# Kernel tuning notes

Measured on AMD Instinct MI355X. Metric: run time of the kernel, lower is better.

The kernel has to match this reference:

```python
import jax, jax.numpy as jnp
import numpy as np

NUM_USER = 50000
NUM_ITEM = 30000
N_NODES = NUM_USER + NUM_ITEM
N_EDGES = 1_000_000
FEAT_DIM = 768
DIM_LATENT = 128
DIM_ID = 64
NEG_SLOPE = 0.01  # F.leaky_relu default


def leaky_relu(x):
    return jnp.where(x >= 0, x, NEG_SLOPE * x)


def l2_normalize(x, eps=1e-12):
    # F.normalize(dim=-1): divide by clamped L2 norm
    n = jnp.sqrt(jnp.sum(x * x, axis=-1, keepdims=True))
    return x / jnp.maximum(n, eps)


def graph_gat(x, W, edge_index, num_nodes):
    """MGAT GraphGAT: x -> x@W, gated inner-product attention, softmax over
    incoming edges per destination node, scatter-add, L2 normalize."""
    x = x @ W                                    # [N, D]
    src = edge_index[0]                          # j (source)
    dst = edge_index[1]                          # i (target)
    x_j = x[src]                                 # [E, D]
    x_i = x[dst]                                 # [E, D]
    inner = jnp.sum(x_i * x_j, axis=-1)          # [E]
    # gate: sigmoid(deg(src)^-0.5 * inner)
    deg = jax.ops.segment_sum(jnp.ones_like(inner), src, num_segments=num_nodes)
    gate = jax.nn.sigmoid(deg[src] ** -0.5 * inner)
    score = inner * gate                         # [E]
    # segment softmax over destination nodes
    smax = jax.ops.segment_max(score, dst, num_segments=num_nodes)
    e = jnp.exp(score - smax[dst])
    denom = jax.ops.segment_sum(e, dst, num_segments=num_nodes)
    alpha = e / (denom[dst] + 1e-16)             # [E]
    out = jax.ops.segment_sum(x_j * alpha[:, None], dst, num_segments=num_nodes)
    return l2_normalize(out)


def setup_inputs() -> dict:
    key = jax.random.key(0)
    ks = jax.random.split(key, 16)

    def xavier(k, shape):
        fan_in, fan_out = shape[0], shape[1]
        std = float(np.sqrt(2.0 / (fan_in + fan_out)))
        return jax.random.normal(k, shape, dtype=jnp.float32) * std

    features = jax.random.normal(ks[0], (NUM_ITEM, FEAT_DIM), dtype=jnp.float32)
    id_embedding = jax.random.normal(ks[1], (N_NODES, DIM_ID), dtype=jnp.float32)
    # edge_index [2, E] with no self-loops (remove_self_loops is then identity)
    src = jax.random.randint(ks[2], (N_EDGES,), 0, N_NODES)
    off = jax.random.randint(ks[3], (N_EDGES,), 1, N_NODES)
    dst = (src + off) % N_NODES
    edge_index = jnp.stack([src, dst]).astype(jnp.int64)

    return {
        "features": features,
        "id_embedding": id_embedding,
        "edge_index": edge_index,
        "preference": xavier(ks[4], (NUM_USER, DIM_LATENT)),
        "mlp_w": xavier(ks[5], (FEAT_DIM, DIM_LATENT)),
        "mlp_b": jnp.zeros((DIM_LATENT,), dtype=jnp.float32),
        "conv1_w": xavier(ks[6], (DIM_LATENT, DIM_LATENT)),
        "lin1_w": xavier(ks[7], (DIM_LATENT, DIM_ID)),
        "lin1_b": jnp.zeros((DIM_ID,), dtype=jnp.float32),
        "g1_w": xavier(ks[8], (DIM_LATENT, DIM_ID)),
        "g1_b": jnp.zeros((DIM_ID,), dtype=jnp.float32),
        "conv2_w": xavier(ks[9], (DIM_ID, DIM_ID)),
        "lin2_w": xavier(ks[10], (DIM_ID, DIM_ID)),
        "lin2_b": jnp.zeros((DIM_ID,), dtype=jnp.float32),
        "g2_w": xavier(ks[11], (DIM_ID, DIM_ID)),
        "g2_b": jnp.zeros((DIM_ID,), dtype=jnp.float32),
    }


def reference(features, id_embedding, edge_index, preference, mlp_w, mlp_b,
              conv1_w, lin1_w, lin1_b, g1_w, g1_b,
              conv2_w, lin2_w, lin2_b, g2_w, g2_b):
    temp_features = jnp.tanh(features @ mlp_w + mlp_b)        # [num_item, dim_latent]
    x = jnp.concatenate([preference, temp_features], axis=0)  # [N, dim_latent]
    x = l2_normalize(x)

    h = leaky_relu(graph_gat(x, conv1_w, edge_index, N_NODES))
    x_hat = leaky_relu(x @ lin1_w + lin1_b) + id_embedding
    x1 = leaky_relu(h @ g1_w + g1_b + x_hat)                  # [N, dim_id]

    h = leaky_relu(graph_gat(x1, conv2_w, edge_index, N_NODES))
    x_hat = leaky_relu(x1 @ lin2_w + lin2_b) + id_embedding
    x2 = leaky_relu(h @ g2_w + g2_b + x_hat)                  # [N, dim_id]

    return jnp.concatenate([x1, x2], axis=1)                  # [N, 2*dim_id]
```

## Files before the change

kernel.cpp:

```cpp
#include <hip/hip_runtime.h>
#include <hip/hip_bf16.h>
#include <math.h>

#define NUM_USER 50000
#define NUM_ITEM 30000
#define N_NODES  80000
#define N_EDGES  1000000
#define FEAT_DIM 768
#define DLAT 128
#define DID  64
#define NEG_SLOPE 0.01f

#define SCAN_NB ((N_NODES + 255) / 256)

__device__ __forceinline__ float leaky(float v) { return v >= 0.f ? v : NEG_SLOPE * v; }

__device__ __forceinline__ float wave_reduce_sum(float v) {
#pragma unroll
    for (int off = 32; off > 0; off >>= 1) v += __shfl_xor(v, off, 64);
    return v;
}

__device__ __forceinline__ unsigned short f2bf(float f) {
    unsigned int u = __float_as_uint(f);
    unsigned int r = u + 0x7fffu + ((u >> 16) & 1u);
    return (unsigned short)(r >> 16);
}
__device__ __forceinline__ float bf2f(unsigned short h) {
    return __uint_as_float(((unsigned int)h) << 16);
}

typedef __attribute__((ext_vector_type(8))) short short8v;
typedef __attribute__((ext_vector_type(4))) float f32x4;

__device__ __forceinline__ void split_store8(
    float4 a, float4 b, unsigned short* dh, unsigned short* dl)
{
    float v[8] = {a.x, a.y, a.z, a.w, b.x, b.y, b.z, b.w};
    unsigned int ph[4], pl[4];
#pragma unroll
    for (int i = 0; i < 4; i++) {
        unsigned short h0 = f2bf(v[2*i]),   l0 = f2bf(v[2*i]   - bf2f(h0));
        unsigned short h1 = f2bf(v[2*i+1]), l1 = f2bf(v[2*i+1] - bf2f(h1));
        ph[i] = (unsigned int)h0 | ((unsigned int)h1 << 16);
        pl[i] = (unsigned int)l0 | ((unsigned int)l1 << 16);
    }
    *(int4*)dh = make_int4((int)ph[0], (int)ph[1], (int)ph[2], (int)ph[3]);
    *(int4*)dl = make_int4((int)pl[0], (int)pl[1], (int)pl[2], (int)pl[3]);
}

template<int KK, int NN>
__global__ __launch_bounds__(256) void wt_prep_g_kernel(
    const float* __restrict__ W, unsigned short* __restrict__ Wh,
    unsigned short* __restrict__ Wl)
{
    int id = blockIdx.x * 256 + threadIdx.x;
    if (id < KK * NN) {
        int n = id / KK, k = id % KK;
        float v = W[(size_t)k * NN + n];
        unsigned short h = f2bf(v);
        Wh[id] = h;
        Wl[id] = f2bf(v - bf2f(h));
    }
}

template<int K, int NC>
__global__ __launch_bounds__(256) void conv_mfma_kernel(
    const float* __restrict__ X, int ldx,
    const unsigned short* __restrict__ Wth, const unsigned short* __restrict__ Wtl,
    float* __restrict__ O, int ldo)
{
    constexpr int NW = NC / 64;
    constexpr int MW = 4 / NW;
    constexpr int WROWS = 64 / MW;
    constexpr int MF = WROWS / 16;
    constexpr int KSTEPS = K / 32;
    constexpr int KP = K + 8;

    __shared__ unsigned short sAh[64][KP];
    __shared__ unsigned short sAl[64][KP];

    const int tid = threadIdx.x;
    const int lane = tid & 63;
    const int w = tid >> 6;
    const int wr = w / NW, wc = w % NW;
    const int r0 = blockIdx.x * 64;

#pragma unroll
    for (int it = 0; it < K / 32; it++) {
        int slot = tid + it * 256;
        int row = slot / (K / 8);
        int k8 = (slot % (K / 8)) * 8;
        const float4* p = (const float4*)(X + (size_t)(r0 + row) * ldx + k8);
        split_store8(p[0], p[1], &sAh[row][k8], &sAl[row][k8]);
    }
    __syncthreads();

    f32x4 acc[MF][4];
#pragma unroll
    for (int m = 0; m < MF; m++)
#pragma unroll
        for (int n = 0; n < 4; n++) acc[m][n] = (f32x4){0.f, 0.f, 0.f, 0.f};

#pragma unroll
    for (int ks = 0; ks < KSTEPS; ks++) {
        int klane = ks * 32 + (lane >> 4) * 8;
        short8v ah[MF], al[MF];
#pragma unroll
        for (int m = 0; m < MF; m++) {
            int row = wr * WROWS + m * 16 + (lane & 15);
            ah[m] = *(const short8v*)&sAh[row][klane];
            al[m] = *(const short8v*)&sAl[row][klane];
        }
#pragma unroll
        for (int n = 0; n < 4; n++) {
            int col = wc * 64 + n * 16 + (lane & 15);
            short8v bh = *(const short8v*)(Wth + (size_t)col * K + klane);
            short8v bl = *(const short8v*)(Wtl + (size_t)col * K + klane);
#pragma unroll
            for (int m = 0; m < MF; m++) {
                acc[m][n] = __builtin_amdgcn_mfma_f32_16x16x32_bf16(ah[m], bh, acc[m][n], 0, 0, 0);
                acc[m][n] = __builtin_amdgcn_mfma_f32_16x16x32_bf16(ah[m], bl, acc[m][n], 0, 0, 0);
                acc[m][n] = __builtin_amdgcn_mfma_f32_16x16x32_bf16(al[m], bh, acc[m][n], 0, 0, 0);
            }
        }
    }

#pragma unroll
    for (int m = 0; m < MF; m++) {
        int rbase = r0 + wr * WROWS + m * 16 + (lane >> 4) * 4;
#pragma unroll
        for (int n = 0; n < 4; n++) {
            int col = wc * 64 + n * 16 + (lane & 15);
#pragma unroll
            for (int q = 0; q < 4; q++)
                O[(size_t)(rbase + q) * ldo + col] = acc[m][n][q];
        }
    }
}

template<int K>
__global__ __launch_bounds__(256) void combine_mfma_kernel(
    const float* __restrict__ H, int ldh,
    const float* __restrict__ X, int ldx,
    const unsigned short* __restrict__ Gth, const unsigned short* __restrict__ Gtl,
    const unsigned short* __restrict__ Lth, const unsigned short* __restrict__ Ltl,
    const float* __restrict__ g_b, const float* __restrict__ lin_b,
    const float* __restrict__ id_emb, float* __restrict__ out, int out_off)
{
    constexpr int KSTEPS = K / 32;
    constexpr int KP = K + 8;

    __shared__ unsigned short sHh[64][KP];
    __shared__ unsigned short sHl[64][KP];
    __shared__ unsigned short sXh[64][KP];
    __shared__ unsigned short sXl[64][KP];

    const int tid = threadIdx.x;
    const int lane = tid & 63;
    const int wr = tid >> 6;
    const int r0 = blockIdx.x * 64;

#pragma unroll
    for (int it = 0; it < K / 32; it++) {
        int slot = tid + it * 256;
        int row = slot / (K / 8);
        int k8 = (slot % (K / 8)) * 8;
        const float4* ph = (const float4*)(H + (size_t)(r0 + row) * ldh + k8);
        split_store8(ph[0], ph[1], &sHh[row][k8], &sHl[row][k8]);
        const float4* px = (const float4*)(X + (size_t)(r0 + row) * ldx + k8);
        split_store8(px[0], px[1], &sXh[row][k8], &sXl[row][k8]);
    }
    __syncthreads();

    f32x4 accG[4], accL[4];
#pragma unroll
    for (int n = 0; n < 4; n++) {
        accG[n] = (f32x4){0.f, 0.f, 0.f, 0.f};
        accL[n] = (f32x4){0.f, 0.f, 0.f, 0.f};
    }

#pragma unroll
    for (int ks = 0; ks < KSTEPS; ks++) {
        int klane = ks * 32 + (lane >> 4) * 8;
        int row = wr * 16 + (lane & 15);
        short8v hh = *(const short8v*)&sHh[row][klane];
        short8v hl = *(const short8v*)&sHl[row][klane];
        short8v xh = *(const short8v*)&sXh[row][klane];
        short8v xl = *(const short8v*)&sXl[row][klane];
#pragma unroll
        for (int n = 0; n < 4; n++) {
            int col = n * 16 + (lane & 15);
            short8v gh = *(const short8v*)(Gth + (size_t)col * K + klane);
            short8v gl = *(const short8v*)(Gtl + (size_t)col * K + klane);
            short8v lh = *(const short8v*)(Lth + (size_t)col * K + klane);
            short8v ll = *(const short8v*)(Ltl + (size_t)col * K + klane);
            accG[n] = __builtin_amdgcn_mfma_f32_16x16x32_bf16(hh, gh, accG[n], 0, 0, 0);
            accG[n] = __builtin_amdgcn_mfma_f32_16x16x32_bf16(hh, gl, accG[n], 0, 0, 0);
            accG[n] = __builtin_amdgcn_mfma_f32_16x16x32_bf16(hl, gh, accG[n], 0, 0, 0);
            accL[n] = __builtin_amdgcn_mfma_f32_16x16x32_bf16(xh, lh, accL[n], 0, 0, 0);
            accL[n] = __builtin_amdgcn_mfma_f32_16x16x32_bf16(xh, ll, accL[n], 0, 0, 0);
            accL[n] = __builtin_amdgcn_mfma_f32_16x16x32_bf16(xl, lh, accL[n], 0, 0, 0);
        }
    }

    int rbase = r0 + wr * 16 + (lane >> 4) * 4;
#pragma unroll
    for (int n = 0; n < 4; n++) {
        int col = n * 16 + (lane & 15);
        float gb = g_b[col], lb = lin_b[col];
#pragma unroll
        for (int q = 0; q < 4; q++) {
            int gr = rbase + q;
            float xhv = leaky(accL[n][q] + lb) + id_emb[(size_t)gr * DID + col];
            float v = leaky(accG[n][q] + gb + xhv);
            out[(size_t)gr * (2 * DID) + out_off + col] = v;
        }
    }
}

__global__ __launch_bounds__(256) void mlp_mfma_kernel(
    const float* __restrict__ F,
    const unsigned short* __restrict__ Wh, const unsigned short* __restrict__ Wl,
    const float* __restrict__ bias, float* __restrict__ xout)
{
    __shared__ unsigned short sAh[64][72];
    __shared__ unsigned short sAl[64][72];
    __shared__ unsigned short sWh[128][72];
    __shared__ unsigned short sWlo[128][72];

    const int tid = threadIdx.x;
    const int lane = tid & 63;
    const int w = tid >> 6;
    const int wr = w >> 1, wc = w & 1;
    const int r0 = blockIdx.x * 64;

    f32x4 acc[2][4];
#pragma unroll
    for (int m = 0; m < 2; m++)
#pragma unroll
        for (int n = 0; n < 4; n++) acc[m][n] = (f32x4){0.f, 0.f, 0.f, 0.f};

    for (int kc = 0; kc < FEAT_DIM; kc += 64) {
#pragma unroll
        for (int it = 0; it < 2; it++) {
            int slot = tid + it * 256;
            int row = slot >> 3;
            int k8 = (slot & 7) * 8;
            int gr = r0 + row;
            float4 a = make_float4(0.f, 0.f, 0.f, 0.f), b = a;
            if (gr < NUM_ITEM) {
                const float4* p = (const float4*)(F + (size_t)gr * FEAT_DIM + kc + k8);
                a = p[0]; b = p[1];
            }
            split_store8(a, b, &sAh[row][k8], &sAl[row][k8]);
        }
#pragma unroll
        for (int it = 0; it < 4; it++) {
            int slot = tid + it * 256;
            int n = slot >> 3;
            int k8 = (slot & 7) * 8;
            *(int4*)&sWh[n][k8]  = *(const int4*)(Wh + (size_t)n * FEAT_DIM + kc + k8);
            *(int4*)&sWlo[n][k8] = *(const int4*)(Wl + (size_t)n * FEAT_DIM + kc + k8);
        }
        __syncthreads();

#pragma unroll
        for (int k0 = 0; k0 < 64; k0 += 32) {
            int klane = k0 + (lane >> 4) * 8;
            short8v ah[2], al[2], bh[4], bl[4];
#pragma unroll
            for (int m = 0; m < 2; m++) {
                int row = wr * 32 + m * 16 + (lane & 15);
                ah[m] = *(const short8v*)&sAh[row][klane];
                al[m] = *(const short8v*)&sAl[row][klane];
            }
#pragma unroll
            for (int n = 0; n < 4; n++) {
                int col = wc * 64 + n * 16 + (lane & 15);
                bh[n] = *(const short8v*)&sWh[col][klane];
                bl[n] = *(const short8v*)&sWlo[col][klane];
            }
#pragma unroll
            for (int m = 0; m < 2; m++)
#pragma unroll
                for (int n = 0; n < 4; n++) {
                    acc[m][n] = __builtin_amdgcn_mfma_f32_16x16x32_bf16(ah[m], bh[n], acc[m][n], 0, 0, 0);
                    acc[m][n] = __builtin_amdgcn_mfma_f32_16x16x32_bf16(ah[m], bl[n], acc[m][n], 0, 0, 0);
                    acc[m][n] = __builtin_amdgcn_mfma_f32_16x16x32_bf16(al[m], bh[n], acc[m][n], 0, 0, 0);
                }
        }
        __syncthreads();
    }

#pragma unroll
    for (int m = 0; m < 2; m++) {
        int rbase = r0 + wr * 32 + m * 16 + (lane >> 4) * 4;
#pragma unroll
        for (int n = 0; n < 4; n++) {
            int col = wc * 64 + n * 16 + (lane & 15);
            float bv = bias[col];
#pragma unroll
            for (int q = 0; q < 4; q++) {
                int gr = rbase + q;
                if (gr < NUM_ITEM)
                    xout[(size_t)gr * DLAT + col] = tanhf(acc[m][n][q] + bv);
            }
        }
    }
}

__global__ __launch_bounds__(256) void l2norm_rows_kernel(float* __restrict__ x)
{
    int wid = blockIdx.x * 4 + (threadIdx.x >> 6);
    if (wid >= N_NODES) return;
    int lane = threadIdx.x & 63;
    float* row = x + (size_t)wid * DLAT;
    float v0 = row[lane], v1 = row[lane + 64];
    float s = wave_reduce_sum(v0 * v0 + v1 * v1);
    float inv = 1.0f / fmaxf(sqrtf(s), 1e-12f);
    row[lane] = v0 * inv;
    row[lane + 64] = v1 * inv;
}

__global__ __launch_bounds__(256) void count_kernel(
    const int* __restrict__ src, const int* __restrict__ dst,
    int* __restrict__ deg_out, int* __restrict__ cnt_in)
{
    int e = blockIdx.x * 256 + threadIdx.x;
    if (e < N_EDGES) {
        atomicAdd(&deg_out[src[e]], 1);
        atomicAdd(&cnt_in[dst[e]], 1);
    }
}

__global__ __launch_bounds__(256) void scan_local_kernel(
    const int* __restrict__ cnt, int* __restrict__ rowptr, int* __restrict__ blocksum)
{
    __shared__ int wsum[4];
    int gid = blockIdx.x * 256 + threadIdx.x;
    int lane = threadIdx.x & 63, w = threadIdx.x >> 6;
    int orig = (gid < N_NODES) ? cnt[gid] : 0;
    int v = orig;
#pragma unroll
    for (int off = 1; off < 64; off <<= 1) {
        int u = __shfl_up(v, off, 64);
        if (lane >= off) v += u;
    }
    if (lane == 63) wsum[w] = v;
    __syncthreads();
    int woff = 0;
#pragma unroll
    for (int i = 0; i < 4; i++) woff += (i < w) ? wsum[i] : 0;
    if (gid < N_NODES) rowptr[gid] = v - orig + woff;
    if (threadIdx.x == 255) blocksum[blockIdx.x] = woff + v;
}

__global__ __launch_bounds__(512) void scan_blocksums_kernel(int* __restrict__ blocksum)
{
    __shared__ int s[512];
    int t = threadIdx.x;
    int orig = (t < SCAN_NB) ? blocksum[t] : 0;
    s[t] = orig;
    __syncthreads();
    for (int off = 1; off < 512; off <<= 1) {
        int u = (t >= off) ? s[t - off] : 0;
        __syncthreads();
        s[t] += u;
        __syncthreads();
    }
    if (t < SCAN_NB) blocksum[t] = s[t] - orig;
}

__global__ __launch_bounds__(256) void scan_add_kernel(
    int* __restrict__ rowptr, const int* __restrict__ blocksum)
{
    int gid = blockIdx.x * 256 + threadIdx.x;
    if (gid < N_NODES) rowptr[gid] += blocksum[blockIdx.x];
    if (gid == 0) rowptr[N_NODES] = N_EDGES;
}

__global__ __launch_bounds__(256) void csr_fill_kernel(
    const int* __restrict__ src, const int* __restrict__ dst,
    const int* __restrict__ rowptr, int* __restrict__ cursor, int* __restrict__ csr_src)
{
    int e = blockIdx.x * 256 + threadIdx.x;
    if (e < N_EDGES) {
        int d = dst[e];
        int slot = rowptr[d] + atomicAdd(&cursor[d], 1);
        csr_src[slot] = src[e];
    }
}

__global__ __launch_bounds__(256) void deg_rsqrt_kernel(
    const int* __restrict__ deg_out, float* __restrict__ rsq)
{
    int n = blockIdx.x * 256 + threadIdx.x;
    if (n < N_NODES) rsq[n] = rsqrtf((float)deg_out[n]);
}

template<int D>
__global__ __launch_bounds__(256) void gat_layer_kernel(
    const float* __restrict__ xw, const int* __restrict__ rowptr,
    const int* __restrict__ csr_src, const float* __restrict__ rsq_deg,
    float* __restrict__ h)
{
    constexpr int SG  = D / 8;
    constexpr int EPC = 64 / SG;
    int wid = blockIdx.x * 4 + (threadIdx.x >> 6);
    if (wid >= N_NODES) return;
    const int lane = threadIdx.x & 63;
    const int g = lane / SG;
    const int t = lane % SG;
    const int start = rowptr[wid], end = rowptr[wid + 1];

    const float* xdp = xw + (size_t)wid * D + 8 * t;
    float4 xd0 = *(const float4*)(xdp);
    float4 xd1 = *(const float4*)(xdp + 4);

    float m = -1e30f, l = 0.f;
    float acc[8];
#pragma unroll
    for (int c = 0; c < 8; c++) acc[c] = 0.f;

    for (int base = start; base < end; base += EPC) {
        int i = base + g;
        bool valid = (i < end);
        int s = valid ? csr_src[i] : 0;
        const float* row = xw + (size_t)s * D + 8 * t;
        float4 a0 = *(const float4*)(row);
        float4 a1 = *(const float4*)(row + 4);
        float p = a0.x * xd0.x + a0.y * xd0.y + a0.z * xd0.z + a0.w * xd0.w
                + a1.x * xd1.x + a1.y * xd1.y + a1.z * xd1.z + a1.w * xd1.w;
#pragma unroll
        for (int off = SG / 2; off > 0; off >>= 1) p += __shfl_xor(p, off, 64);
        float rsd = valid ? rsq_deg[s] : 1.f;
        float gate = 1.0f / (1.0f + __expf(-(p * rsd)));
        float sc = valid ? p * gate : -1e30f;
        float mnew = fmaxf(m, sc);
        float scale = __expf(m - mnew);
        float w = valid ? __expf(sc - mnew) : 0.f;
        l = l * scale + w;
        acc[0] = acc[0] * scale + w * a0.x;
        acc[1] = acc[1] * scale + w * a0.y;
        acc[2] = acc[2] * scale + w * a0.z;
        acc[3] = acc[3] * scale + w * a0.w;
        acc[4] = acc[4] * scale + w * a1.x;
        acc[5] = acc[5] * scale + w * a1.y;
        acc[6] = acc[6] * scale + w * a1.z;
        acc[7] = acc[7] * scale + w * a1.w;
        m = mnew;
    }

#pragma unroll
    for (int off = SG; off < 64; off <<= 1) {
        float mo = __shfl_xor(m, off, 64);
        float lo = __shfl_xor(l, off, 64);
        float mnew = fmaxf(m, mo);
        float s1 = __expf(m - mnew), s2 = __expf(mo - mnew);
        l = l * s1 + lo * s2;
#pragma unroll
        for (int c = 0; c < 8; c++) {
            float ao = __shfl_xor(acc[c], off, 64);
            acc[c] = acc[c] * s1 + ao * s2;
        }
        m = mnew;
    }

    float invl = 1.0f / (l + 1e-16f);
    float ss = 0.f;
#pragma unroll
    for (int c = 0; c < 8; c++) { acc[c] *= invl; ss += acc[c] * acc[c]; }
#pragma unroll
    for (int off = SG / 2; off > 0; off >>= 1) ss += __shfl_xor(ss, off, 64);
    float inv = 1.0f / fmaxf(sqrtf(ss), 1e-12f);

    if (g == 0) {
        float4 o0, o1;
        o0.x = leaky(acc[0] * inv); o0.y = leaky(acc[1] * inv);
        o0.z = leaky(acc[2] * inv); o0.w = leaky(acc[3] * inv);
        o1.x = leaky(acc[4] * inv); o1.y = leaky(acc[5] * inv);
        o1.z = leaky(acc[6] * inv); o1.w = leaky(acc[7] * inv);
        float* op = h + (size_t)wid * D + 8 * t;
        *(float4*)(op) = o0;
        *(float4*)(op + 4) = o1;
    }
}

extern "C" void kernel_launch(void* const* d_in, const int* in_sizes, int n_in,
                              void* d_out, int out_size, void* d_ws, size_t ws_size,
                              hipStream_t stream)
{
    const float* features = (const float*)d_in[0];
    const float* id_emb   = (const float*)d_in[1];
    const int*   ei       = (const int*)d_in[2];
    const float* pref     = (const float*)d_in[3];
    const float* mlp_w    = (const float*)d_in[4];
    const float* mlp_b    = (const float*)d_in[5];
    const float* conv1_w  = (const float*)d_in[6];
    const float* lin1_w   = (const float*)d_in[7];
    const float* lin1_b   = (const float*)d_in[8];
    const float* g1_w     = (const float*)d_in[9];
    const float* g1_b     = (const float*)d_in[10];
    const float* conv2_w  = (const float*)d_in[11];
    const float* lin2_w   = (const float*)d_in[12];
    const float* lin2_b   = (const float*)d_in[13];
    const float* g2_w     = (const float*)d_in[14];
    const float* g2_b     = (const float*)d_in[15];
    const int* src = ei;
    const int* dst = ei + N_EDGES;
    float* out = (float*)d_out;

    float* x       = (float*)d_ws;
    float* xw      = x   + (size_t)N_NODES * DLAT;
    float* gat     = xw  + (size_t)N_NODES * DLAT;
    int*   deg_out = (int*)(gat + (size_t)N_NODES * DLAT);
    int*   cnt     = deg_out + N_NODES;
    int*   rowptr  = cnt + N_NODES;
    int*   csr_src = rowptr + N_NODES + 1;
    int*   blocksum = csr_src + N_EDGES;
    float* rsq_deg = (float*)cnt;
    unsigned short* mlpWh = (unsigned short*)gat;
    unsigned short* mlpWl = mlpWh + (size_t)FEAT_DIM * DLAT;
    unsigned short* wbase = (unsigned short*)(
        (((uintptr_t)(blocksum + SCAN_NB)) + 15) & ~(uintptr_t)15);
    unsigned short* wc1h = wbase;
    unsigned short* wc1l = wc1h + 16384;
    unsigned short* wl1h = wc1l + 16384;
    unsigned short* wl1l = wl1h + 8192;
    unsigned short* wg1h = wl1l + 8192;
    unsigned short* wg1l = wg1h + 8192;
    unsigned short* wc2h = wg1l + 8192;
    unsigned short* wc2l = wc2h + 4096;
    unsigned short* wl2h = wc2l + 4096;
    unsigned short* wl2l = wl2h + 4096;
    unsigned short* wg2h = wl2l + 4096;
    unsigned short* wg2l = wg2h + 4096;

    wt_prep_g_kernel<FEAT_DIM, DLAT><<<384, 256, 0, stream>>>(mlp_w, mlpWh, mlpWl);
    wt_prep_g_kernel<DLAT, DLAT><<<64, 256, 0, stream>>>(conv1_w, wc1h, wc1l);
    wt_prep_g_kernel<DLAT, DID><<<32, 256, 0, stream>>>(lin1_w, wl1h, wl1l);
    wt_prep_g_kernel<DLAT, DID><<<32, 256, 0, stream>>>(g1_w, wg1h, wg1l);
    wt_prep_g_kernel<DID, DID><<<16, 256, 0, stream>>>(conv2_w, wc2h, wc2l);
    wt_prep_g_kernel<DID, DID><<<16, 256, 0, stream>>>(lin2_w, wl2h, wl2l);
    wt_prep_g_kernel<DID, DID><<<16, 256, 0, stream>>>(g2_w, wg2h, wg2l);

    hipMemsetAsync(deg_out, 0, N_NODES * sizeof(int), stream);
    hipMemsetAsync(cnt, 0, N_NODES * sizeof(int), stream);
    count_kernel<<<(N_EDGES + 255) / 256, 256, 0, stream>>>(src, dst, deg_out, cnt);
    scan_local_kernel<<<SCAN_NB, 256, 0, stream>>>(cnt, rowptr, blocksum);
    scan_blocksums_kernel<<<1, 512, 0, stream>>>(blocksum);
    scan_add_kernel<<<SCAN_NB, 256, 0, stream>>>(rowptr, blocksum);
    hipMemsetAsync(cnt, 0, N_NODES * sizeof(int), stream);
    csr_fill_kernel<<<(N_EDGES + 255) / 256, 256, 0, stream>>>(src, dst, rowptr, cnt, csr_src);
    deg_rsqrt_kernel<<<(N_NODES + 255) / 256, 256, 0, stream>>>(deg_out, rsq_deg);

    hipMemcpyAsync(x, pref, (size_t)NUM_USER * DLAT * sizeof(float),
                   hipMemcpyDeviceToDevice, stream);
    mlp_mfma_kernel<<<(NUM_ITEM + 63) / 64, 256, 0, stream>>>(
        features, mlpWh, mlpWl, mlp_b, x + (size_t)NUM_USER * DLAT);
    l2norm_rows_kernel<<<(N_NODES + 3) / 4, 256, 0, stream>>>(x);

    conv_mfma_kernel<DLAT, DLAT><<<N_NODES / 64, 256, 0, stream>>>(
        x, DLAT, wc1h, wc1l, xw, DLAT);
    gat_layer_kernel<DLAT><<<(N_NODES + 3) / 4, 256, 0, stream>>>(
        xw, rowptr, csr_src, rsq_deg, gat);
    combine_mfma_kernel<DLAT><<<N_NODES / 64, 256, 0, stream>>>(
        gat, DLAT, x, DLAT, wg1h, wg1l, wl1h, wl1l, g1_b, lin1_b, id_emb, out, 0);

    conv_mfma_kernel<DID, DID><<<N_NODES / 64, 256, 0, stream>>>(
        out, 2 * DID, wc2h, wc2l, xw, DID);
    gat_layer_kernel<DID><<<(N_NODES + 3) / 4, 256, 0, stream>>>(
        xw, rowptr, csr_src, rsq_deg, gat);
    combine_mfma_kernel<DID><<<N_NODES / 64, 256, 0, stream>>>(
        gat, DID, out, 2 * DID, wg2h, wg2l, wl2h, wl2l, g2_b, lin2_b, id_emb, out, DID);
}
```

Baseline: 517.8 us.

## Store projected node features in bf16 and fuse small setup kernels

Measured after the change: 488.7 us. -5.6%, faster.

```diff
diff --git a/kernel.cpp b/kernel.cpp
--- a/kernel.cpp
+++ b/kernel.cpp
@@ -33,6 +33,14 @@
 typedef __attribute__((ext_vector_type(8))) short short8v;
 typedef __attribute__((ext_vector_type(4))) float f32x4;
 
+__device__ __forceinline__ void unpack8(int4 v, float* f) {
+    unsigned int u;
+    u = (unsigned int)v.x; f[0] = __uint_as_float(u << 16); f[1] = __uint_as_float(u & 0xFFFF0000u);
+    u = (unsigned int)v.y; f[2] = __uint_as_float(u << 16); f[3] = __uint_as_float(u & 0xFFFF0000u);
+    u = (unsigned int)v.z; f[4] = __uint_as_float(u << 16); f[5] = __uint_as_float(u & 0xFFFF0000u);
+    u = (unsigned int)v.w; f[6] = __uint_as_float(u << 16); f[7] = __uint_as_float(u & 0xFFFF0000u);
+}
+
 __device__ __forceinline__ void split_store8(
     float4 a, float4 b, unsigned short* dh, unsigned short* dl)
 {
@@ -49,26 +57,44 @@
     *(int4*)dl = make_int4((int)pl[0], (int)pl[1], (int)pl[2], (int)pl[3]);
 }
 
-template<int KK, int NN>
-__global__ __launch_bounds__(256) void wt_prep_g_kernel(
-    const float* __restrict__ W, unsigned short* __restrict__ Wh,
-    unsigned short* __restrict__ Wl)
+__device__ __forceinline__ void prep_one(int id, const float* W, int KK, int NN,
+                                         unsigned short* Wh, unsigned short* Wl)
+{
+    int n = id / KK, k = id - n * KK;
+    float v = W[(size_t)k * NN + n];
+    unsigned short h = f2bf(v);
+    Wh[id] = h;
+    Wl[id] = f2bf(v - bf2f(h));
+}
+
+__global__ __launch_bounds__(256) void wt_prep_all_kernel(
+    const float* __restrict__ mlp_w, const float* __restrict__ c1,
+    const float* __restrict__ l1, const float* __restrict__ g1,
+    const float* __restrict__ c2, const float* __restrict__ l2,
+    const float* __restrict__ g2,
+    unsigned short* __restrict__ mlpWh, unsigned short* __restrict__ mlpWl,
+    unsigned short* __restrict__ wc1h, unsigned short* __restrict__ wc1l,
+    unsigned short* __restrict__ wl1h, unsigned short* __restrict__ wl1l,
+    unsigned short* __restrict__ wg1h, unsigned short* __restrict__ wg1l,
+    unsigned short* __restrict__ wc2h, unsigned short* __restrict__ wc2l,
+    unsigned short* __restrict__ wl2h, unsigned short* __restrict__ wl2l,
+    unsigned short* __restrict__ wg2h, unsigned short* __restrict__ wg2l)
 {
     int id = blockIdx.x * 256 + threadIdx.x;
-    if (id < KK * NN) {
-        int n = id / KK, k = id % KK;
-        float v = W[(size_t)k * NN + n];
-        unsigned short h = f2bf(v);
-        Wh[id] = h;
-        Wl[id] = f2bf(v - bf2f(h));
-    }
+    if (id < 98304)       prep_one(id,          mlp_w, FEAT_DIM, DLAT, mlpWh, mlpWl);
+    else if (id < 114688) prep_one(id - 98304,  c1, DLAT, DLAT, wc1h, wc1l);
+    else if (id < 122880) prep_one(id - 114688, l1, DLAT, DID,  wl1h, wl1l);
+    else if (id < 131072) prep_one(id - 122880, g1, DLAT, DID,  wg1h, wg1l);
+    else if (id < 135168) prep_one(id - 131072, c2, DID,  DID,  wc2h, wc2l);
+    else if (id < 139264) prep_one(id - 135168, l2, DID,  DID,  wl2h, wl2l);
+    else if (id < 143360) prep_one(id - 139264, g2, DID,  DID,  wg2h, wg2l);
 }
 
 template<int K, int NC>
 __global__ __launch_bounds__(256) void conv_mfma_kernel(
     const float* __restrict__ X, int ldx,
     const unsigned short* __restrict__ Wth, const unsigned short* __restrict__ Wtl,
-    float* __restrict__ O, int ldo)
+    unsigned short* __restrict__ O, int ldo)
 {
     constexpr int NW = NC / 64;
     constexpr int MW = 4 / NW;
@@ -134,7 +160,7 @@
             int col = wc * 64 + n * 16 + (lane & 15);
 #pragma unroll
             for (int q = 0; q < 4; q++)
-                O[(size_t)(rbase + q) * ldo + col] = acc[m][n][q];
+                O[(size_t)(rbase + q) * ldo + col] = f2bf(acc[m][n][q]);
         }
     }
 }
@@ -310,17 +336,20 @@
     }
 }
 
-__global__ __launch_bounds__(256) void l2norm_rows_kernel(float* __restrict__ x)
+__global__ __launch_bounds__(256) void normcopy_kernel(
+    const float* __restrict__ pref, float* __restrict__ x)
 {
     int wid = blockIdx.x * 4 + (threadIdx.x >> 6);
     if (wid >= N_NODES) return;
     int lane = threadIdx.x & 63;
-    float* row = x + (size_t)wid * DLAT;
-    float v0 = row[lane], v1 = row[lane + 64];
+    const float* srow = (wid < NUM_USER) ? (pref + (size_t)wid * DLAT)
+                                         : (x + (size_t)wid * DLAT);
+    float v0 = srow[lane], v1 = srow[lane + 64];
     float s = wave_reduce_sum(v0 * v0 + v1 * v1);
     float inv = 1.0f / fmaxf(sqrtf(s), 1e-12f);
-    row[lane] = v0 * inv;
-    row[lane + 64] = v1 * inv;
+    float* drow = x + (size_t)wid * DLAT;
+    drow[lane] = v0 * inv;
+    drow[lane + 64] = v1 * inv;
 }
 
 __global__ __launch_bounds__(256) void count_kernel(
@@ -372,11 +401,16 @@
     if (t < SCAN_NB) blocksum[t] = s[t] - orig;
 }
 
-__global__ __launch_bounds__(256) void scan_add_kernel(
-    int* __restrict__ rowptr, const int* __restrict__ blocksum)
+__global__ __launch_bounds__(256) void scan_add_plus_kernel(
+    int* __restrict__ rowptr, const int* __restrict__ blocksum,
+    int* __restrict__ cnt, const int* __restrict__ deg_out, float* __restrict__ rsq)
 {
     int gid = blockIdx.x * 256 + threadIdx.x;
-    if (gid < N_NODES) rowptr[gid] += blocksum[blockIdx.x];
+    if (gid < N_NODES) {
+        rowptr[gid] += blocksum[blockIdx.x];
+        cnt[gid] = 0;
+        rsq[gid] = rsqrtf((float)deg_out[gid]);
+    }
     if (gid == 0) rowptr[N_NODES] = N_EDGES;
 }
 
@@ -392,16 +426,9 @@
     }
 }
 
-__global__ __launch_bounds__(256) void deg_rsqrt_kernel(
-    const int* __restrict__ deg_out, float* __restrict__ rsq)
-{
-    int n = blockIdx.x * 256 + threadIdx.x;
-    if (n < N_NODES) rsq[n] = rsqrtf((float)deg_out[n]);
-}
-
 template<int D>
 __global__ __launch_bounds__(256) void gat_layer_kernel(
-    const float* __restrict__ xw, const int* __restrict__ rowptr,
+    const unsigned short* __restrict__ xw, const int* __restrict__ rowptr,
     const int* __restrict__ csr_src, const float* __restrict__ rsq_deg,
     float* __restrict__ h)
 {
@@ -414,9 +441,11 @@
     const int t = lane % SG;
     const int start = rowptr[wid], end = rowptr[wid + 1];
 
-    const float* xdp = xw + (size_t)wid * D + 8 * t;
-    float4 xd0 = *(const float4*)(xdp);
-    float4 xd1 = *(const float4*)(xdp + 4);
+    float xd[8];
+    {
+        int4 v = *(const int4*)(xw + (size_t)wid * D + 8 * t);
+        unpack8(v, xd);
+    }
 
     float m = -1e30f, l = 0.f;
     float acc[8];
@@ -427,11 +456,11 @@
         int i = base + g;
         bool valid = (i < end);
         int s = valid ? csr_src[i] : 0;
-        const float* row = xw + (size_t)s * D + 8 * t;
-        float4 a0 = *(const float4*)(row);
-        float4 a1 = *(const float4*)(row + 4);
-        float p = a0.x * xd0.x + a0.y * xd0.y + a0.z * xd0.z + a0.w * xd0.w
-                + a1.x * xd1.x + a1.y * xd1.y + a1.z * xd1.z + a1.w * xd1.w;
+        int4 av = *(const int4*)(xw + (size_t)s * D + 8 * t);
+        float a[8];
+        unpack8(av, a);
+        float p = a[0]*xd[0] + a[1]*xd[1] + a[2]*xd[2] + a[3]*xd[3]
+                + a[4]*xd[4] + a[5]*xd[5] + a[6]*xd[6] + a[7]*xd[7];
 #pragma unroll
         for (int off = SG / 2; off > 0; off >>= 1) p += __shfl_xor(p, off, 64);
         float rsd = valid ? rsq_deg[s] : 1.f;
@@ -441,14 +470,8 @@
         float scale = __expf(m - mnew);
         float w = valid ? __expf(sc - mnew) : 0.f;
         l = l * scale + w;
-        acc[0] = acc[0] * scale + w * a0.x;
-        acc[1] = acc[1] * scale + w * a0.y;
-        acc[2] = acc[2] * scale + w * a0.z;
-        acc[3] = acc[3] * scale + w * a0.w;
-        acc[4] = acc[4] * scale + w * a1.x;
-        acc[5] = acc[5] * scale + w * a1.y;
-        acc[6] = acc[6] * scale + w * a1.z;
-        acc[7] = acc[7] * scale + w * a1.w;
+#pragma unroll
+        for (int c = 0; c < 8; c++) acc[c] = acc[c] * scale + w * a[c];
         m = mnew;
     }
 
@@ -511,19 +534,19 @@
     const int* dst = ei + N_EDGES;
     float* out = (float*)d_out;
 
-    float* x       = (float*)d_ws;
-    float* xw      = x   + (size_t)N_NODES * DLAT;
-    float* gat     = xw  + (size_t)N_NODES * DLAT;
-    int*   deg_out = (int*)(gat + (size_t)N_NODES * DLAT);
-    int*   cnt     = deg_out + N_NODES;
-    int*   rowptr  = cnt + N_NODES;
-    int*   csr_src = rowptr + N_NODES + 1;
+    float* x        = (float*)d_ws;
+    unsigned short* xwb = (unsigned short*)(x + (size_t)N_NODES * DLAT);
+    float* gat      = (float*)(xwb + (size_t)N_NODES * DLAT);
+    int*   deg_out  = (int*)(gat + (size_t)N_NODES * DLAT);
+    int*   cnt      = deg_out + N_NODES;
+    int*   rowptr   = cnt + N_NODES;
+    int*   csr_src  = rowptr + N_NODES + 1;
     int*   blocksum = csr_src + N_EDGES;
-    float* rsq_deg = (float*)cnt;
+    float* rsq_deg  = (float*)(blocksum + SCAN_NB);
     unsigned short* mlpWh = (unsigned short*)gat;
     unsigned short* mlpWl = mlpWh + (size_t)FEAT_DIM * DLAT;
     unsigned short* wbase = (unsigned short*)(
-        (((uintptr_t)(blocksum + SCAN_NB)) + 15) & ~(uintptr_t)15);
+        (((uintptr_t)(rsq_deg + N_NODES)) + 15) & ~(uintptr_t)15);
     unsigned short* wc1h = wbase;
     unsigned short* wc1l = wc1h + 16384;
     unsigned short* wl1h = wc1l + 16384;
@@ -537,41 +560,33 @@
     unsigned short* wg2h = wl2l + 4096;
     unsigned short* wg2l = wg2h + 4096;
 
-    wt_prep_g_kernel<FEAT_DIM, DLAT><<<384, 256, 0, stream>>>(mlp_w, mlpWh, mlpWl);
-    wt_prep_g_kernel<DLAT, DLAT><<<64, 256, 0, stream>>>(conv1_w, wc1h, wc1l);
-    wt_prep_g_kernel<DLAT, DID><<<32, 256, 0, stream>>>(lin1_w, wl1h, wl1l);
-    wt_prep_g_kernel<DLAT, DID><<<32, 256, 0, stream>>>(g1_w, wg1h, wg1l);
-    wt_prep_g_kernel<DID, DID><<<16, 256, 0, stream>>>(conv2_w, wc2h, wc2l);
-    wt_prep_g_kernel<DID, DID><<<16, 256, 0, stream>>>(lin2_w, wl2h, wl2l);
-    wt_prep_g_kernel<DID, DID><<<16, 256, 0, stream>>>(g2_w, wg2h, wg2l);
-
-    hipMemsetAsync(deg_out, 0, N_NODES * sizeof(int), stream);
-    hipMemsetAsync(cnt, 0, N_NODES * sizeof(int), stream);
+    hipMemsetAsync(deg_out, 0, 2 * N_NODES * sizeof(int), stream);
+    wt_prep_all_kernel<<<560, 256, 0, stream>>>(
+        mlp_w, conv1_w, lin1_w, g1_w, conv2_w, lin2_w, g2_w,
+        mlpWh, mlpWl, wc1h, wc1l, wl1h, wl1l, wg1h, wg1l,
+        wc2h, wc2l, wl2h, wl2l, wg2h, wg2l);
+
     count_kernel<<<(N_EDGES + 255) / 256, 256, 0, stream>>>(src, dst, deg_out, cnt);
     scan_local_kernel<<<SCAN_NB, 256, 0, stream>>>(cnt, rowptr, blocksum);
     scan_blocksums_kernel<<<1, 512, 0, stream>>>(blocksum);
-    scan_add_kernel<<<SCAN_NB, 256, 0, stream>>>(rowptr, blocksum);
-    hipMemsetAsync(cnt, 0, N_NODES * sizeof(int), stream);
+    scan_add_plus_kernel<<<SCAN_NB, 256, 0, stream>>>(rowptr, blocksum, cnt, deg_out, rsq_deg);
     csr_fill_kernel<<<(N_EDGES + 255) / 256, 256, 0, stream>>>(src, dst, rowptr, cnt, csr_src);
-    deg_rsqrt_kernel<<<(N_NODES + 255) / 256, 256, 0, stream>>>(deg_out, rsq_deg);
-
-    hipMemcpyAsync(x, pref, (size_t)NUM_USER * DLAT * sizeof(float),
-                   hipMemcpyDeviceToDevice, stream);
+
     mlp_mfma_kernel<<<(NUM_ITEM + 63) / 64, 256, 0, stream>>>(
         features, mlpWh, mlpWl, mlp_b, x + (size_t)NUM_USER * DLAT);
-    l2norm_rows_kernel<<<(N_NODES + 3) / 4, 256, 0, stream>>>(x);
+    normcopy_kernel<<<(N_NODES + 3) / 4, 256, 0, stream>>>(pref, x);
 
     conv_mfma_kernel<DLAT, DLAT><<<N_NODES / 64, 256, 0, stream>>>(
-        x, DLAT, wc1h, wc1l, xw, DLAT);
+        x, DLAT, wc1h, wc1l, xwb, DLAT);
     gat_layer_kernel<DLAT><<<(N_NODES + 3) / 4, 256, 0, stream>>>(
-        xw, rowptr, csr_src, rsq_deg, gat);
+        xwb, rowptr, csr_src, rsq_deg, gat);
     combine_mfma_kernel<DLAT><<<N_NODES / 64, 256, 0, stream>>>(
         gat, DLAT, x, DLAT, wg1h, wg1l, wl1h, wl1l, g1_b, lin1_b, id_emb, out, 0);
 
     conv_mfma_kernel<DID, DID><<<N_NODES / 64, 256, 0, stream>>>(
-        out, 2 * DID, wc2h, wc2l, xw, DID);
+        out, 2 * DID, wc2h, wc2l, xwb, DID);
     gat_layer_kernel<DID><<<(N_NODES + 3) / 4, 256, 0, stream>>>(
-        xw, rowptr, csr_src, rsq_deg, gat);
+        xwb, rowptr, csr_src, rsq_deg, gat);
     combine_mfma_kernel<DID><<<N_NODES / 64, 256, 0, stream>>>(
         gat, DID, out, 2 * DID, wg2h, wg2l, wl2h, wl2l, g2_b, lin2_b, id_emb, out, DID);
 }
```
